# Kernel tuning notes

Hardware: AMD Instinct MI355X
Metric: run time of the kernel (lower is better)

## Reference

```python
import jax, jax.numpy as jnp
import numpy as np

NUM_HEADS = 12
ALPHA = 0.5
TANH_CLIP = 5.0


def setup_inputs() -> dict:
    key = jax.random.key(0)
    k1, k2, k3, k4, k5 = jax.random.split(key, 5)
    B, N, C = 8, 1024, 768
    x = jax.random.normal(k1, (B, N, C), dtype=jnp.float32)
    # qkv: Linear(C -> 3C), proj: Linear(C -> C); torch stores weight as [out, in]
    s = 1.0 / np.sqrt(C)
    qkv_w = jax.random.normal(k2, (3 * C, C), dtype=jnp.float32) * s
    qkv_b = jax.random.normal(k3, (3 * C,), dtype=jnp.float32) * 0.02
    proj_w = jax.random.normal(k4, (C, C), dtype=jnp.float32) * s
    proj_b = jax.random.normal(k5, (C,), dtype=jnp.float32) * 0.02
    return {"x": x, "qkv_w": qkv_w, "qkv_b": qkv_b, "proj_w": proj_w, "proj_b": proj_b}


def reference(x, qkv_w, qkv_b, proj_w, proj_b):
    B, N, C = x.shape
    H = NUM_HEADS
    D = C // H
    scale = D ** -0.5
    # qkv projection -> [B, N, 3, H, D] -> q/k/v each [B, H, N, D]
    qkv = (x @ qkv_w.T + qkv_b).reshape(B, N, 3, H, D)
    qkv = jnp.transpose(qkv, (2, 0, 3, 1, 4))
    q, k, v = qkv[0], qkv[1], qkv[2]
    # pre-softmax scores [B, H, N, N]
    scores = jnp.einsum("bhnd,bhmd->bhnm", q * scale, k)
    scores_t = jnp.swapaxes(scores, -2, -1)
    scores_sym = 0.5 * (scores + scores_t)
    scores_asym = 0.5 * (scores - scores_t)
    scores = scores_sym + ALPHA * scores_asym
    # gamma_mode == 'approx'
    gamma = np.sqrt((1.0 + ALPHA ** 2) / 2.0)
    scores = scores / gamma
    # tanh clip
    scores = TANH_CLIP * jnp.tanh(scores / TANH_CLIP)
    attn = jax.nn.softmax(scores, axis=-1)
    out = jnp.einsum("bhnm,bhmd->bhnd", attn, v)  # [B, H, N, D]
    out = jnp.transpose(out, (0, 2, 1, 3)).reshape(B, N, C)
    return out @ proj_w.T + proj_b
```

## Files before the change

kernel.cpp:

```cpp
#include <hip/hip_runtime.h>
#include <hip/hip_bf16.h>
#include <stdint.h>

typedef unsigned short u16;
typedef __attribute__((ext_vector_type(8))) short bf16x8;
typedef __attribute__((ext_vector_type(4))) float f32x4;

#define LDS_AS(p) ((__attribute__((address_space(3))) void*)(p))
#define GLB_AS(p) ((__attribute__((address_space(1))) void*)(p))

__device__ __forceinline__ u16 f2bf(float f) {
  union { float f; uint32_t u; } v; v.f = f;
  uint32_t u = v.u;
  u += 0x7fffu + ((u >> 16) & 1u);
  return (u16)(u >> 16);
}

__device__ __forceinline__ float exp2_fast(float x) {
  float r;
  asm("v_exp_f32 %0, %1" : "=v"(r) : "v"(x));
  return r;
}

__device__ __forceinline__ float bits2f(uint32_t u) {
  union { uint32_t u; float f; } v; v.u = u; return v.f;
}
__device__ __forceinline__ uint32_t f2bits(float f) {
  union { float f; uint32_t u; } v; v.f = f; return v.u;
}
__device__ __forceinline__ uint32_t pack_hi16(uint32_t lo_src, uint32_t hi_src) {
  return __builtin_amdgcn_perm(hi_src, lo_src, 0x07060302u);
}

__device__ __forceinline__ void cvt8(const float* __restrict__ s, u16* __restrict__ d) {
  const float4* sv = (const float4*)s;
  float4 a = sv[0], b = sv[1];
  uint4 o;
  o.x = (uint32_t)f2bf(a.x) | ((uint32_t)f2bf(a.y) << 16);
  o.y = (uint32_t)f2bf(a.z) | ((uint32_t)f2bf(a.w) << 16);
  o.z = (uint32_t)f2bf(b.x) | ((uint32_t)f2bf(b.y) << 16);
  o.w = (uint32_t)f2bf(b.z) | ((uint32_t)f2bf(b.w) << 16);
  *(uint4*)d = o;
}

__global__ __launch_bounds__(256) void k_convert(
    const float* __restrict__ x, const float* __restrict__ wq, const float* __restrict__ wp,
    u16* __restrict__ xb, u16* __restrict__ wqb, u16* __restrict__ wpb) {
  int tid = blockIdx.x * 256 + threadIdx.x;
  int np  = gridDim.x * 256;
  for (int i = tid; i < (8192*768)/8; i += np) cvt8(x  + (size_t)i*8, xb  + (size_t)i*8);
  for (int i = tid; i < (2304*768)/8; i += np) cvt8(wq + (size_t)i*8, wqb + (size_t)i*8);
  for (int i = tid; i < (768*768)/8;  i += np) cvt8(wp + (size_t)i*8, wpb + (size_t)i*8);
}

template<bool SWAP>
__device__ __forceinline__ void gemm_core(const u16* __restrict__ A,
                                          const u16* __restrict__ B,
                                          u16* As, u16* Bs,
                                          int rowA0, int rowB0,
                                          f32x4 acc[4][4]) {
  const int t  = threadIdx.x;
  const int lane = t & 63;
  const int wv = t >> 6;
  const int wr = wv >> 1, wc = wv & 1;
  const int lr = lane & 15, lg = lane >> 4;

#pragma unroll 1
  for (int kt = 0; kt < 24; ++kt) {
    const int k0 = kt * 32;
    __syncthreads();
#pragma unroll
    for (int p = 0; p < 2; ++p) {
      int idx = p * 256 + t;
      int row = idx >> 2;
      int cc  = (idx & 3) ^ ((row >> 1) & 3);
      __builtin_amdgcn_global_load_lds(GLB_AS(A + (size_t)(rowA0 + row) * 768 + k0 + cc * 8),
                                       LDS_AS(As + idx * 8), 16, 0, 0);
    }
#pragma unroll
    for (int p = 0; p < 2; ++p) {
      int idx = p * 256 + t;
      int row = idx >> 2;
      int cc  = (idx & 3) ^ ((row >> 1) & 3);
      __builtin_amdgcn_global_load_lds(GLB_AS(B + (size_t)(rowB0 + row) * 768 + k0 + cc * 8),
                                       LDS_AS(Bs + idx * 8), 16, 0, 0);
    }
    asm volatile("s_waitcnt vmcnt(0)" ::: "memory");
    __syncthreads();

    bf16x8 af[4], bf_[4];
#pragma unroll
    for (int mi = 0; mi < 4; ++mi) {
      int row = wr * 64 + mi * 16 + lr;
      int cc  = lg ^ ((row >> 1) & 3);
      af[mi] = *(const bf16x8*)(As + row * 32 + cc * 8);
    }
#pragma unroll
    for (int ni = 0; ni < 4; ++ni) {
      int row = wc * 64 + ni * 16 + lr;
      int cc  = lg ^ ((row >> 1) & 3);
      bf_[ni] = *(const bf16x8*)(Bs + row * 32 + cc * 8);
    }
#pragma unroll
    for (int mi = 0; mi < 4; ++mi)
#pragma unroll
      for (int ni = 0; ni < 4; ++ni) {
        if (SWAP)
          acc[mi][ni] = __builtin_amdgcn_mfma_f32_16x16x32_bf16(bf_[ni], af[mi], acc[mi][ni], 0, 0, 0);
        else
          acc[mi][ni] = __builtin_amdgcn_mfma_f32_16x16x32_bf16(af[mi], bf_[ni], acc[mi][ni], 0, 0, 0);
      }
  }
}

__global__ __launch_bounds__(256) void k_gemm_qkv(
    const u16* __restrict__ Aq, const u16* __restrict__ Bw, const float* __restrict__ bias,
    u16* __restrict__ Qh, u16* __restrict__ Kh, u16* __restrict__ Vt) {
  __shared__ u16 As[128 * 32];
  __shared__ u16 Bs[128 * 32];
  int bid = blockIdx.x;
  int wg  = (bid & 7) * 144 + (bid >> 3);
  int bx  = wg % 18, by = wg / 18;

  const int t = threadIdx.x, lane = t & 63, wv = t >> 6;
  const int wr = wv >> 1, wc = wv & 1, lr = lane & 15, lg = lane >> 4;
  const int tsec = bx / 6;
  const int colBase = bx * 128 + wc * 64;

  const float gam = 0.7905694150420949f;
  const float rC1 = __builtin_sqrtf(0.57707801636f);
  const float sc1 = __builtin_sqrtf(0.09375f / gam) * rC1;
  const float sc2 = __builtin_sqrtf(0.03125f / gam) * rC1;

  f32x4 acc[4][4];
#pragma unroll
  for (int mi = 0; mi < 4; ++mi)
#pragma unroll
    for (int ni = 0; ni < 4; ++ni) acc[mi][ni] = (f32x4){0.f, 0.f, 0.f, 0.f};

  if (tsec < 2) {
    gemm_core<true>(Aq, Bw, As, Bs, by * 128, bx * 128, acc);

    float4 bv4[4];
#pragma unroll
    for (int ni = 0; ni < 4; ++ni)
      bv4[ni] = *(const float4*)(bias + colBase + ni * 16 + lg * 4);

#pragma unroll
    for (int mi = 0; mi < 4; ++mi) {
      int n = by * 128 + wr * 64 + mi * 16 + lr;
      int b = n >> 10, nn = n & 1023;
#pragma unroll
      for (int ni = 0; ni < 4; ++ni) {
        int fs = colBase - tsec * 768 + ni * 16 + lg * 4;
        int h = fs >> 6, d = fs & 63;
        size_t rowq = ((size_t)(b * 12 + h) * 1024 + nn) * 128;
        float v0 = acc[mi][ni][0] + bv4[ni].x;
        float v1 = acc[mi][ni][1] + bv4[ni].y;
        float v2 = acc[mi][ni][2] + bv4[ni].z;
        float v3 = acc[mi][ni][3] + bv4[ni].w;
        uint2 wq_, wk_;
        wq_.x = (uint32_t)f2bf(v0 * sc1) | ((uint32_t)f2bf(v1 * sc1) << 16);
        wq_.y = (uint32_t)f2bf(v2 * sc1) | ((uint32_t)f2bf(v3 * sc1) << 16);
        wk_.x = (uint32_t)f2bf(v0 * sc2) | ((uint32_t)f2bf(v1 * sc2) << 16);
        wk_.y = (uint32_t)f2bf(v2 * sc2) | ((uint32_t)f2bf(v3 * sc2) << 16);
        if (tsec == 0) {
          *(uint2*)(Qh + rowq + d)      = wq_;
          *(uint2*)(Kh + rowq + 64 + d) = wk_;
        } else {
          *(uint2*)(Kh + rowq + d)      = wq_;
          *(uint2*)(Qh + rowq + 64 + d) = wk_;
        }
      }
    }
  } else {
    gemm_core<false>(Aq, Bw, As, Bs, by * 128, bx * 128, acc);

    float bv[4];
#pragma unroll
    for (int ni = 0; ni < 4; ++ni) bv[ni] = bias[colBase + ni * 16 + lr];

#pragma unroll
    for (int mi = 0; mi < 4; ++mi) {
      int tok0 = by * 128 + wr * 64 + mi * 16 + lg * 4;
      int b = tok0 >> 10, n0 = tok0 & 1023;
#pragma unroll
      for (int ni = 0; ni < 4; ++ni) {
        int fs = colBase - 2 * 768 + ni * 16 + lr;
        int h = fs >> 6, d = fs & 63;
        float v0 = acc[mi][ni][0] + bv[ni];
        float v1 = acc[mi][ni][1] + bv[ni];
        float v2 = acc[mi][ni][2] + bv[ni];
        float v3 = acc[mi][ni][3] + bv[ni];
        uint2 w;
        w.x = (uint32_t)f2bf(v0) | ((uint32_t)f2bf(v1) << 16);
        w.y = (uint32_t)f2bf(v2) | ((uint32_t)f2bf(v3) << 16);
        *(uint2*)(Vt + ((size_t)((b * 12 + h) * 64 + d)) * 1024 + n0) = w;
      }
    }
  }
}

__global__ __launch_bounds__(256, 3) void k_attn(
    const u16* __restrict__ Qh, const u16* __restrict__ Kh, const u16* __restrict__ Vt,
    u16* __restrict__ attn) {
  __shared__ u16 Ks[3][32 * 128];
  __shared__ u16 Vs[3][64 * 32];
  __shared__ u16 Ps[4][32 * 40];

  int bid = blockIdx.x;
  int wg = (bid & 7) * 96 + (bid >> 3);
  int bh = wg >> 3, qb = wg & 7;
  int b = bh / 12, h = bh % 12;

  const int t = threadIdx.x, lane = t & 63, wv = t >> 6;
  const int lr = lane & 15, lg = lane >> 4;

  const size_t khb = (size_t)bh * 1024 * 128;
  const size_t vtb = (size_t)bh * 64 * 1024;

  bf16x8 qf[2][4];
  {
    const u16* qp = Qh + ((size_t)bh * 1024 + qb * 128 + wv * 32 + lr) * 128 + lg * 8;
#pragma unroll
    for (int it = 0; it < 2; ++it)
#pragma unroll
      for (int kk = 0; kk < 4; ++kk)
        qf[it][kk] = *(const bf16x8*)(qp + it * 16 * 128 + kk * 32);
  }
  asm volatile("s_waitcnt vmcnt(0)" ::: "memory");
  __builtin_amdgcn_sched_barrier(0);

#define STAGE(KT, BUF)                                                                         \
  {                                                                                            \
    _Pragma("unroll")                                                                          \
    for (int p = 0; p < 2; ++p) {                                                              \
      int idx = p * 256 + t;                                                                   \
      int row = idx >> 4;                                                                      \
      int cc  = (idx & 15) ^ (row & 7);                                                        \
      __builtin_amdgcn_global_load_lds(GLB_AS(Kh + khb + (size_t)((KT) * 32 + row) * 128 + cc * 8), \
                                       LDS_AS(Ks[BUF] + idx * 8), 16, 0, 0);                   \
    }                                                                                          \
    {                                                                                          \
      int d = t >> 2;                                                                          \
      int g = (t & 3) ^ ((d + (d >> 2)) & 3);                                                  \
      __builtin_amdgcn_global_load_lds(GLB_AS(Vt + vtb + (size_t)d * 1024 + (KT) * 32 + g * 8),\
                                       LDS_AS(Vs[BUF] + t * 8), 16, 0, 0);                     \
    }                                                                                          \
  }

  STAGE(0, 0);
  STAGE(1, 1);

  f32x4 acc_o[4][2];
#pragma unroll
  for (int dt = 0; dt < 4; ++dt)
#pragma unroll
    for (int it = 0; it < 2; ++it) acc_o[dt][it] = (f32x4){0.f, 0.f, 0.f, 0.f};
  float dsum[2] = {0.f, 0.f};

  u16* pw = Ps[wv];
  const float C2 = -14.4269504089f;

  int cur = 0, stg = 2;
#pragma unroll 1
  for (int kt = 0; kt < 32; ++kt) {
    if (kt < 31) {
      asm volatile("s_waitcnt vmcnt(3)" ::: "memory");
    } else {
      asm volatile("s_waitcnt vmcnt(0)" ::: "memory");
    }
    __builtin_amdgcn_sched_barrier(0);
    __builtin_amdgcn_s_barrier();
    __builtin_amdgcn_sched_barrier(0);

    if (kt < 30) STAGE(kt + 2, stg);

    const u16* K0 = Ks[cur];
    f32x4 accs[2][2];
#pragma unroll
    for (int jt = 0; jt < 2; ++jt)
#pragma unroll
      for (int it = 0; it < 2; ++it) accs[jt][it] = (f32x4){0.f, 0.f, 0.f, 0.f};
    __builtin_amdgcn_s_setprio(1);
#pragma unroll
    for (int jt = 0; jt < 2; ++jt) {
#pragma unroll
      for (int kk = 0; kk < 4; ++kk) {
        int row = jt * 16 + lr;
        int cc  = (kk * 4 + lg) ^ (row & 7);
        bf16x8 kf = *(const bf16x8*)(K0 + row * 128 + cc * 8);
#pragma unroll
        for (int it = 0; it < 2; ++it)
          accs[jt][it] = __builtin_amdgcn_mfma_f32_16x16x32_bf16(kf, qf[it][kk], accs[jt][it], 0, 0, 0);
      }
    }
    __builtin_amdgcn_s_setprio(0);

#pragma unroll
    for (int jt = 0; jt < 2; ++jt) {
#pragma unroll
      for (int it = 0; it < 2; ++it) {
        float p0 = exp2_fast(C2 * __builtin_amdgcn_rcpf(exp2_fast(accs[jt][it][0]) + 1.0f));
        float p1 = exp2_fast(C2 * __builtin_amdgcn_rcpf(exp2_fast(accs[jt][it][1]) + 1.0f));
        float p2 = exp2_fast(C2 * __builtin_amdgcn_rcpf(exp2_fast(accs[jt][it][2]) + 1.0f));
        float p3 = exp2_fast(C2 * __builtin_amdgcn_rcpf(exp2_fast(accs[jt][it][3]) + 1.0f));
        uint32_t a0 = f2bits(p0), a1 = f2bits(p1), a2 = f2bits(p2), a3 = f2bits(p3);
        uint2 w;
        w.x = pack_hi16(a0, a1);
        w.y = pack_hi16(a2, a3);
        dsum[it] += (bits2f(a0 & 0xFFFF0000u) + bits2f(a1 & 0xFFFF0000u))
                  + (bits2f(a2 & 0xFFFF0000u) + bits2f(a3 & 0xFFFF0000u));
        *(uint2*)(pw + (it * 16 + lr) * 40 + jt * 16 + lg * 4) = w;
      }
    }

    asm volatile("" ::: "memory");

    {
      const u16* V0 = Vs[cur];
      bf16x8 pa[2];
#pragma unroll
      for (int it = 0; it < 2; ++it)
        pa[it] = *(const bf16x8*)(pw + (it * 16 + lr) * 40 + lg * 8);
      __builtin_amdgcn_s_setprio(1);
#pragma unroll
      for (int dt = 0; dt < 4; ++dt) {
        int row = dt * 16 + lr;
        int ph  = lg ^ ((row + (row >> 2)) & 3);
        bf16x8 vf = *(const bf16x8*)(V0 + row * 32 + ph * 8);
#pragma unroll
        for (int it = 0; it < 2; ++it)
          acc_o[dt][it] = __builtin_amdgcn_mfma_f32_16x16x32_bf16(vf, pa[it], acc_o[dt][it], 0, 0, 0);
      }
      __builtin_amdgcn_s_setprio(0);
    }

    cur = (cur == 2) ? 0 : cur + 1;
    stg = (stg == 2) ? 0 : stg + 1;
  }
#undef STAGE

  float rinv[2];
#pragma unroll
  for (int it = 0; it < 2; ++it) {
    float v = dsum[it];
    v += __shfl_xor(v, 16);
    v += __shfl_xor(v, 32);
    rinv[it] = __builtin_amdgcn_rcpf(v);
  }

#pragma unroll
  for (int dt = 0; dt < 4; ++dt) {
#pragma unroll
    for (int it = 0; it < 2; ++it) {
      float v0 = acc_o[dt][it][0] * rinv[it];
      float v1 = acc_o[dt][it][1] * rinv[it];
      float v2 = acc_o[dt][it][2] * rinv[it];
      float v3 = acc_o[dt][it][3] * rinv[it];
      uint2 w;
      w.x = (uint32_t)f2bf(v0) | ((uint32_t)f2bf(v1) << 16);
      w.y = (uint32_t)f2bf(v2) | ((uint32_t)f2bf(v3) << 16);
      int n = qb * 128 + wv * 32 + it * 16 + lr;
      *(uint2*)(attn + ((size_t)(b * 1024 + n)) * 768 + h * 64 + dt * 16 + lg * 4) = w;
    }
  }
}

__global__ __launch_bounds__(256) void k_gemm_proj(
    const u16* __restrict__ Ain, const u16* __restrict__ Bw, const float* __restrict__ bias,
    float* __restrict__ out) {
  __shared__ u16 As[128 * 32];
  __shared__ u16 Bs[128 * 32];
  int bid = blockIdx.x;
  int wg  = (bid & 7) * 48 + (bid >> 3);
  int bx  = wg % 6, by = wg / 6;

  f32x4 acc[4][4];
#pragma unroll
  for (int mi = 0; mi < 4; ++mi)
#pragma unroll
    for (int ni = 0; ni < 4; ++ni) acc[mi][ni] = (f32x4){0.f, 0.f, 0.f, 0.f};

  gemm_core<false>(Ain, Bw, As, Bs, by * 128, bx * 128, acc);

  const int t = threadIdx.x, lane = t & 63, wv = t >> 6;
  const int wr = wv >> 1, wc = wv & 1, lr = lane & 15, lg = lane >> 4;
  const int col0 = bx * 128 + wc * 64;

  float bv[4];
#pragma unroll
  for (int ni = 0; ni < 4; ++ni) bv[ni] = bias[col0 + ni * 16 + lr];

#pragma unroll
  for (int mi = 0; mi < 4; ++mi) {
    int tok0 = by * 128 + wr * 64 + mi * 16 + lg * 4;
#pragma unroll
    for (int ni = 0; ni < 4; ++ni) {
      int col = col0 + ni * 16 + lr;
#pragma unroll
      for (int r = 0; r < 4; ++r) {
        out[(size_t)(tok0 + r) * 768 + col] = acc[mi][ni][r] + bv[ni];
      }
    }
  }
}

extern "C" void kernel_launch(void* const* d_in, const int* in_sizes, int n_in,
                              void* d_out, int out_size, void* d_ws, size_t ws_size,
                              hipStream_t stream) {
  (void)in_sizes; (void)n_in; (void)out_size;
  const float* x      = (const float*)d_in[0];
  const float* qkv_w  = (const float*)d_in[1];
  const float* qkv_b  = (const float*)d_in[2];
  const float* proj_w = (const float*)d_in[3];
  const float* proj_b = (const float*)d_in[4];
  float* out = (float*)d_out;

  uint8_t* ws = (uint8_t*)d_ws;
  u16* xb  = (u16*)(ws + 0);
  u16* wqb = (u16*)(ws + 12582912);
  u16* wpb = (u16*)(ws + 16121856);
  u16* Qh  = (u16*)(ws + 17301504);
  u16* Kh  = (u16*)(ws + 42467328);
  u16* Vt  = (u16*)(ws + 80216064);
  if (ws_size < 92798976) return;

  u16* attnb = xb;

  k_convert<<<1024, 256, 0, stream>>>(x, qkv_w, proj_w, xb, wqb, wpb);
  k_gemm_qkv<<<1152, 256, 0, stream>>>(xb, wqb, qkv_b, Qh, Kh, Vt);
  k_attn<<<768, 256, 0, stream>>>(Qh, Kh, Vt, attnb);
  k_gemm_proj<<<384, 256, 0, stream>>>(attnb, wpb, proj_b, out);
}
```

Measured before the change: 155.9 us.

## Double-buffer LDS tiles in shared GEMM core to overlap loads with MFMA

The shared GEMM core used by the QKV and output projection kernels now keeps two LDS buffers for each operand. While the current K-slice is read and fed to MFMA, the next slice is prefetched with global_load_lds, and the explicit vmcnt(0) wait is removed. The aim is to hide global-to-LDS latency behind compute and drop one barrier per iteration. This doubles LDS use per block. Correctness relies on the barrier or compiler-inserted waitcnt ensuring the current buffer's async loads have landed before the ds_reads.

```diff
diff --git a/kernel.cpp b/kernel.cpp
--- a/kernel.cpp
+++ b/kernel.cpp
@@ -65,41 +65,49 @@
   const int wr = wv >> 1, wc = wv & 1;
   const int lr = lane & 15, lg = lane >> 4;
 
+#define GSTAGE(KT, BUF)                                                                         \
+  {                                                                                             \
+    _Pragma("unroll")                                                                           \
+    for (int p = 0; p < 2; ++p) {                                                               \
+      int idx = p * 256 + t;                                                                    \
+      int row = idx >> 2;                                                                       \
+      int cc  = (idx & 3) ^ ((row >> 1) & 3);                                                   \
+      __builtin_amdgcn_global_load_lds(GLB_AS(A + (size_t)(rowA0 + row) * 768 + (KT) * 32 + cc * 8), \
+                                       LDS_AS(As + (BUF) * 4096 + idx * 8), 16, 0, 0);          \
+    }                                                                                           \
+    _Pragma("unroll")                                                                           \
+    for (int p = 0; p < 2; ++p) {                                                               \
+      int idx = p * 256 + t;                                                                    \
+      int row = idx >> 2;                                                                       \
+      int cc  = (idx & 3) ^ ((row >> 1) & 3);                                                   \
+      __builtin_amdgcn_global_load_lds(GLB_AS(B + (size_t)(rowB0 + row) * 768 + (KT) * 32 + cc * 8), \
+                                       LDS_AS(Bs + (BUF) * 4096 + idx * 8), 16, 0, 0);          \
+    }                                                                                           \
+  }
+
+  GSTAGE(0, 0);
+
 #pragma unroll 1
   for (int kt = 0; kt < 24; ++kt) {
-    const int k0 = kt * 32;
+    const int cur = kt & 1;
     __syncthreads();
-#pragma unroll
-    for (int p = 0; p < 2; ++p) {
-      int idx = p * 256 + t;
-      int row = idx >> 2;
-      int cc  = (idx & 3) ^ ((row >> 1) & 3);
-      __builtin_amdgcn_global_load_lds(GLB_AS(A + (size_t)(rowA0 + row) * 768 + k0 + cc * 8),
-                                       LDS_AS(As + idx * 8), 16, 0, 0);
-    }
-#pragma unroll
-    for (int p = 0; p < 2; ++p) {
-      int idx = p * 256 + t;
-      int row = idx >> 2;
-      int cc  = (idx & 3) ^ ((row >> 1) & 3);
-      __builtin_amdgcn_global_load_lds(GLB_AS(B + (size_t)(rowB0 + row) * 768 + k0 + cc * 8),
-                                       LDS_AS(Bs + idx * 8), 16, 0, 0);
-    }
-    asm volatile("s_waitcnt vmcnt(0)" ::: "memory");
-    __syncthreads();
-
+
+    if (kt < 23) GSTAGE(kt + 1, cur ^ 1);
+
+    const u16* Ab = As + cur * 4096;
+    const u16* Bb = Bs + cur * 4096;
     bf16x8 af[4], bf_[4];
 #pragma unroll
     for (int mi = 0; mi < 4; ++mi) {
       int row = wr * 64 + mi * 16 + lr;
       int cc  = lg ^ ((row >> 1) & 3);
-      af[mi] = *(const bf16x8*)(As + row * 32 + cc * 8);
+      af[mi] = *(const bf16x8*)(Ab + row * 32 + cc * 8);
     }
 #pragma unroll
     for (int ni = 0; ni < 4; ++ni) {
       int row = wc * 64 + ni * 16 + lr;
       int cc  = lg ^ ((row >> 1) & 3);
-      bf_[ni] = *(const bf16x8*)(Bs + row * 32 + cc * 8);
+      bf_[ni] = *(const bf16x8*)(Bb + row * 32 + cc * 8);
     }
 #pragma unroll
     for (int mi = 0; mi < 4; ++mi)
@@ -111,13 +119,14 @@
           acc[mi][ni] = __builtin_amdgcn_mfma_f32_16x16x32_bf16(af[mi], bf_[ni], acc[mi][ni], 0, 0, 0);
       }
   }
+#undef GSTAGE
 }
 
 __global__ __launch_bounds__(256) void k_gemm_qkv(
     const u16* __restrict__ Aq, const u16* __restrict__ Bw, const float* __restrict__ bias,
     u16* __restrict__ Qh, u16* __restrict__ Kh, u16* __restrict__ Vt) {
-  __shared__ u16 As[128 * 32];
-  __shared__ u16 Bs[128 * 32];
+  __shared__ u16 As[2 * 128 * 32];
+  __shared__ u16 Bs[2 * 128 * 32];
   int bid = blockIdx.x;
   int wg  = (bid & 7) * 144 + (bid >> 3);
   int bx  = wg % 18, by = wg / 18;
@@ -370,8 +379,8 @@
 __global__ __launch_bounds__(256) void k_gemm_proj(
     const u16* __restrict__ Ain, const u16* __restrict__ Bw, const float* __restrict__ bias,
     float* __restrict__ out) {
-  __shared__ u16 As[128 * 32];
-  __shared__ u16 Bs[128 * 32];
+  __shared__ u16 As[2 * 128 * 32];
+  __shared__ u16 Bs[2 * 128 * 32];
   int bid = blockIdx.x;
   int wg  = (bid & 7) * 48 + (bid >> 3);
   int bx  = wg % 6, by = wg / 6;
```

Measured after the change: 150.0 us. 3.8% less time.
